# Kernel tuning notes

Measured on AMD Instinct MI355X. Metric: run time of the kernel, lower is better.

## Reference

```python
import jax, jax.numpy as jnp
import numpy as np

B, T, H_IMG, HID, ACT = 128, 100, 72, 512, 2


def _conv(x, w, b, stride, pad):
    y = jax.lax.conv_general_dilated(
        x, w, (stride, stride), [(pad, pad), (pad, pad)],
        dimension_numbers=('NCHW', 'OIHW', 'NCHW'))
    return y + b[None, :, None, None]


def _encode(images, cw1, cb1, cw2, cb2, cw3, cb3, fw1, fb1, fw2, fb2, fw3, fb3):
    relu = jax.nn.relu
    x = relu(_conv(images, cw1, cb1, 3, 2))   # [B,64,24,24]
    x = relu(_conv(x, cw2, cb2, 3, 2))        # [B,64,9,9]
    x = relu(_conv(x, cw3, cb3, 3, 2))        # [B,64,4,4]
    x = x.reshape(x.shape[0], -1)             # [B,1024]
    x = relu(x @ fw1.T + fb1)
    x = relu(x @ fw2.T + fb2)
    return x @ fw3.T + fb3                    # [B,512]


def _gru(actions, h0, w_ih, w_hh, b_ih, b_hh):
    # precompute input projections for all steps: [T,B,3H]
    gi = jnp.einsum('btd,gd->tbg', actions, w_ih) + b_ih

    def step(h, gi_t):
        gh = h @ w_hh.T + b_hh
        i_r, i_i, i_n = jnp.split(gi_t, 3, axis=-1)
        h_r, h_i, h_n = jnp.split(gh, 3, axis=-1)
        r = jax.nn.sigmoid(i_r + h_r)
        z = jax.nn.sigmoid(i_i + h_i)
        n = jnp.tanh(i_n + r * h_n)
        hy = n + z * (h - n)
        return hy, hy

    hT, outs = jax.lax.scan(step, h0, gi)
    return jnp.transpose(outs, (1, 0, 2)), hT  # batch_first output


def setup_inputs() -> dict:
    key = jax.random.key(0)
    ks = jax.random.split(key, 16)
    s = 0.05
    return {
        'images': jax.random.normal(ks[0], (B, 3, H_IMG, H_IMG), jnp.float32),
        'actions': jax.random.normal(ks[1], (B, T, ACT), jnp.float32),
        'cw1': jax.random.normal(ks[2], (64, 3, 5, 5), jnp.float32) * s,
        'cb1': jax.random.normal(ks[3], (64,), jnp.float32) * s,
        'cw2': jax.random.normal(ks[4], (64, 64, 3, 3), jnp.float32) * s,
        'cb2': jax.random.normal(ks[5], (64,), jnp.float32) * s,
        'cw3': jax.random.normal(ks[6], (64, 64, 3, 3), jnp.float32) * s,
        'cb3': jax.random.normal(ks[7], (64,), jnp.float32) * s,
        'fw1': jax.random.normal(ks[8], (1024, 1024), jnp.float32) * 0.02,
        'fb1': jax.random.normal(ks[9], (1024,), jnp.float32) * 0.02,
        'fw2': jax.random.normal(ks[10], (512, 1024), jnp.float32) * 0.02,
        'fb2': jax.random.normal(ks[11], (512,), jnp.float32) * 0.02,
        'fw3': jax.random.normal(ks[12], (512, 512), jnp.float32) * 0.02,
        'fb3': jax.random.normal(ks[13], (512,), jnp.float32) * 0.02,
        'w_ih': jax.random.normal(ks[14], (3 * HID, ACT), jnp.float32) * 0.05,
        'w_hh': jax.random.normal(ks[15], (3 * HID, HID), jnp.float32) * 0.04,
        'b_ih': jnp.zeros((3 * HID,), jnp.float32),
        'b_hh': jnp.zeros((3 * HID,), jnp.float32),
    }


def reference(images, actions, cw1, cb1, cw2, cb2, cw3, cb3,
              fw1, fb1, fw2, fb2, fw3, fb3, w_ih, w_hh, b_ih, b_hh):
    # Encode the start image to a 512-d representation (BigBasicConv),
    # then integrate the action sequence with the hand-rolled GRU,
    # initial hidden state = start representation.
    h0 = _encode(images, cw1, cb1, cw2, cb2, cw3, cb3,
                 fw1, fb1, fw2, fb2, fw3, fb3)
    output, hT = _gru(actions, h0, w_ih, w_hh, b_ih, b_hh)
    return output, hT
```

## Files before the change

kernel.cpp:

```cpp
#include <hip/hip_runtime.h>
#include <cstdint>

#define BB   128
#define TT   100
#define HID  512

typedef __attribute__((ext_vector_type(4))) float f32x4;
typedef __attribute__((ext_vector_type(2))) float f32x2;
typedef __attribute__((ext_vector_type(8))) short short8;
typedef __attribute__((ext_vector_type(4))) short short4_t;

__device__ __forceinline__ short f2bf(float x) {
  unsigned u = __float_as_uint(x);
  unsigned r = (u + 0x7fffu + ((u >> 16) & 1u)) >> 16;
  return (short)r;
}
__device__ __forceinline__ float bf2f(short s) {
  return __uint_as_float(((unsigned)(unsigned short)s) << 16);
}

__global__ __launch_bounds__(256) void wsplit_k(const float* __restrict__ w,
                                                unsigned short* __restrict__ hi,
                                                unsigned short* __restrict__ lo,
                                                int nq) {
  int i = blockIdx.x * 256 + threadIdx.x;
  const int stride = gridDim.x * 256;
  for (; i < nq; i += stride) {
    f32x4 v = *(const f32x4*)(w + 4 * (long)i);
    short4_t h, l;
    #pragma unroll
    for (int c = 0; c < 4; c++) {
      short hh = f2bf(v[c]); h[c] = hh; l[c] = f2bf(v[c] - bf2f(hh));
    }
    *(short4_t*)(hi + 4 * (long)i) = h;
    *(short4_t*)(lo + 4 * (long)i) = l;
  }
}


__global__ __launch_bounds__(192) void conv1_k(const float* __restrict__ in,
                                               const float* __restrict__ w,
                                               const float* __restrict__ bias,
                                               float* __restrict__ out) {
  const int b = blockIdx.x / 24, oy = blockIdx.x % 24;
  __shared__ __attribute__((aligned(16))) float in_s[3][5][76];
  __shared__ __attribute__((aligned(16))) float ws[64][76];
  const int tid = threadIdx.x;
  for (int i = tid; i < 3 * 5 * 76; i += 192) {
    int ic = i / 380, rem = i % 380, r = rem / 76, p = rem % 76;
    int iy = oy * 3 + r - 2, ix = p - 2;
    in_s[ic][r][p] = (iy >= 0 && iy < 72 && ix >= 0 && ix < 72)
                       ? in[((long)(b * 3 + ic) * 72 + iy) * 72 + ix] : 0.f;
  }
  for (int i = tid; i < 64 * 75; i += 192) ws[i / 75][i % 75] = w[i];
  __syncthreads();

  const int ox2 = tid % 12;
  const int og = tid / 12;
  float strip[15][8];
  #pragma unroll
  for (int ic = 0; ic < 3; ic++)
    #pragma unroll
    for (int ky = 0; ky < 5; ky++) {
      const float* bp = &in_s[ic][ky][6 * ox2];
      #pragma unroll
      for (int h = 0; h < 4; h++) {
        f32x2 u = *(const f32x2*)(bp + 2 * h);
        strip[ic * 5 + ky][2 * h] = u[0];
        strip[ic * 5 + ky][2 * h + 1] = u[1];
      }
    }

  #pragma unroll
  for (int j = 0; j < 4; j++) {
    const int oc = og + 16 * j;
    float s0 = bias[oc], s1 = bias[oc];
    const float* wrow = ws[oc];
    #pragma unroll
    for (int k4 = 0; k4 < 18; k4++) {
      f32x4 wq = *(const f32x4*)(wrow + 4 * k4);
      #pragma unroll
      for (int q = 0; q < 4; q++) {
        const int k = 4 * k4 + q, i5 = k / 5, kx = k % 5;
        s0 += strip[i5][kx] * wq[q];
        s1 += strip[i5][kx + 3] * wq[q];
      }
    }
    s0 += strip[14][2] * wrow[72]; s1 += strip[14][5] * wrow[72];
    s0 += strip[14][3] * wrow[73]; s1 += strip[14][6] * wrow[73];
    s0 += strip[14][4] * wrow[74]; s1 += strip[14][7] * wrow[74];
    long o = ((long)(b * 64 + oc) * 24 + oy) * 24 + 2 * ox2;
    out[o] = fmaxf(s0, 0.f);
    out[o + 1] = fmaxf(s1, 0.f);
  }
}

template <int IC, int IH, int IW, int OC, int OH, int OW>
__global__ void convs3(const float* __restrict__ in, const float* __restrict__ w,
                       const float* __restrict__ bias, float* __restrict__ out) {
  const int b = blockIdx.x / OH, oy = blockIdx.x % OH;
  constexpr int PW = 3 * OW;
  constexpr int NT = (OC / 2) * OW;
  __shared__ __attribute__((aligned(16))) float in_s[8][3][PW];
  __shared__ __attribute__((aligned(16))) float w_s[OC][100];
  const int tid = threadIdx.x;
  const int oc = tid / OW, ox = tid % OW;
  float s0 = bias[oc], s1 = bias[oc + OC / 2];
  for (int cc = 0; cc < IC; cc += 8) {
    __syncthreads();
    for (int i = tid; i < 8 * 3 * PW; i += NT) {
      int ic = i / (3 * PW), r = (i / PW) % 3, p = i % PW;
      int iy = oy * 3 - 2 + r, ix = p - 2;
      in_s[ic][r][p] = (iy >= 0 && iy < IH && ix >= 0 && ix < IW)
                         ? in[((long)(b * IC + cc + ic) * IH + iy) * IW + ix] : 0.f;
    }
    for (int i = tid; i < OC * 8 * 9; i += NT) {
      int o = i / 72, r = i % 72;
      w_s[o][(r / 9) * 12 + (r % 9)] = w[(long)(o * IC + cc + r / 9) * 9 + r % 9];
    }
    __syncthreads();
    #pragma unroll
    for (int ic = 0; ic < 8; ic++) {
      const float* wr0 = &w_s[oc][ic * 12];
      const float* wr1 = &w_s[oc + OC / 2][ic * 12];
      f32x4 wa = *(const f32x4*)wr0, wb = *(const f32x4*)(wr0 + 4);
      f32x4 va = *(const f32x4*)wr1, vb = *(const f32x4*)(wr1 + 4);
      float wA[9] = {wa[0], wa[1], wa[2], wa[3], wb[0], wb[1], wb[2], wb[3], wr0[8]};
      float wB[9] = {va[0], va[1], va[2], va[3], vb[0], vb[1], vb[2], vb[3], wr1[8]};
      #pragma unroll
      for (int ky = 0; ky < 3; ky++)
        #pragma unroll
        for (int kx = 0; kx < 3; kx++) {
          float iv = in_s[ic][ky][ox * 3 + kx];
          s0 += iv * wA[ky * 3 + kx];
          s1 += iv * wB[ky * 3 + kx];
        }
    }
  }
  out[((long)(b * OC + oc) * OH + oy) * OW + ox] = fmaxf(s0, 0.f);
  out[((long)(b * OC + oc + OC / 2) * OH + oy) * OW + ox] = fmaxf(s1, 0.f);
}

template <int K, int N, bool RELU>
__global__ __launch_bounds__(128) void fc_mfma(const float* __restrict__ A,
                                               const unsigned short* __restrict__ wh,
                                               const unsigned short* __restrict__ wl,
                                               const float* __restrict__ bias,
                                               float* __restrict__ C) {
  const int nb = N / 32;
  const int rb = (blockIdx.x / nb) * 16, cb = (blockIdx.x % nb) * 32;
  __shared__ __attribute__((aligned(16))) short A_hi[16][K + 8];
  __shared__ __attribute__((aligned(16))) short A_lo[16][K + 8];
  const int tid = threadIdx.x;
  const int wv = tid >> 6, lane = tid & 63, n16 = lane & 15, quad = lane >> 4;

  for (int i = tid; i < 16 * (K / 4); i += 128) {
    int row = i / (K / 4), q = i % (K / 4);
    f32x4 v = *(const f32x4*)(A + (long)(rb + row) * K + 4 * q);
    short4_t sh, sl;
    #pragma unroll
    for (int c = 0; c < 4; c++) {
      short hh = f2bf(v[c]); sh[c] = hh; sl[c] = f2bf(v[c] - bf2f(hh));
    }
    *(short4_t*)&A_hi[row][4 * q] = sh;
    *(short4_t*)&A_lo[row][4 * q] = sl;
  }
  __syncthreads();

  const int col = cb + wv * 16 + n16;
  f32x4 a0 = {0.f, 0.f, 0.f, 0.f}, a1 = a0, a2 = a0;
  constexpr int NP = K / 512;
  #pragma unroll 1
  for (int p = 0; p < NP; p++) {
    short8 fh[16], fl[16];
    const unsigned short* wb0 = wh + (long)col * K + p * 512 + quad * 8;
    const unsigned short* wb1 = wl + (long)col * K + p * 512 + quad * 8;
    #pragma unroll
    for (int ks = 0; ks < 16; ks++) {
      fh[ks] = *(const short8*)(wb0 + ks * 32);
      fl[ks] = *(const short8*)(wb1 + ks * 32);
    }
    #pragma unroll
    for (int ks = 0; ks < 16; ks++) {
      short8 ah = *(const short8*)&A_hi[n16][p * 512 + ks * 32 + quad * 8];
      short8 al = *(const short8*)&A_lo[n16][p * 512 + ks * 32 + quad * 8];
      a0 = __builtin_amdgcn_mfma_f32_16x16x32_bf16(ah, fh[ks], a0, 0, 0, 0);
      a1 = __builtin_amdgcn_mfma_f32_16x16x32_bf16(al, fh[ks], a1, 0, 0, 0);
      a2 = __builtin_amdgcn_mfma_f32_16x16x32_bf16(ah, fl[ks], a2, 0, 0, 0);
    }
  }
  const float bv = bias[col];
  #pragma unroll
  for (int r = 0; r < 4; r++) {
    float v = a0[r] + a1[r] + a2[r] + bv;
    if (RELU) v = fmaxf(v, 0.f);
    C[(long)(rb + quad * 4 + r) * N + col] = v;
  }
}

__global__ __launch_bounds__(192, 1) void gru_k(
    const float* __restrict__ actions, const float* __restrict__ w_ih,
    const float* __restrict__ w_hh, const float* __restrict__ b_ih,
    const float* __restrict__ b_hh, const float* __restrict__ h0,
    float* __restrict__ out, float* __restrict__ hT, unsigned* __restrict__ bar) {
  const int bg = blockIdx.x >> 5;
  const int hg = blockIdx.x & 31;
  const int tid = threadIdx.x;
  const int wv = tid >> 6;
  const int lane = tid & 63;
  const int n16 = lane & 15;
  const int quad = lane >> 4;

  __shared__ short h_hi[16][520];
  __shared__ short h_lo[16][520];
  __shared__ float act_s[16][2 * TT];
  __shared__ float gh_s[3][16][17];
  __shared__ float bih_s[48], bhh_s[48], wih0_s[48], wih1_s[48];

  short8 whi[16], wlo[16];
  {
    const int grow = wv * HID + hg * 16 + n16;
    const float* wr = w_hh + (long)grow * HID + quad * 8;
    #pragma unroll
    for (int ks = 0; ks < 16; ks++) {
      f32x4 v0 = *(const f32x4*)(wr + ks * 32);
      f32x4 v1 = *(const f32x4*)(wr + ks * 32 + 4);
      short8 hi, lo;
      #pragma unroll
      for (int j = 0; j < 4; j++) {
        short h1 = f2bf(v0[j]); hi[j] = h1;     lo[j] = f2bf(v0[j] - bf2f(h1));
        short h2 = f2bf(v1[j]); hi[j + 4] = h2; lo[j + 4] = f2bf(v1[j] - bf2f(h2));
      }
      whi[ks] = hi; wlo[ks] = lo;
    }
  }
  for (int i = tid; i < 48; i += 192) {
    int row = (i >> 4) * HID + hg * 16 + (i & 15);
    bih_s[i] = b_ih[row];
    bhh_s[i] = b_hh[row];
    wih0_s[i] = w_ih[row * 2];
    wih1_s[i] = w_ih[row * 2 + 1];
  }
  for (int i = tid; i < 16 * 2 * TT; i += 192) {
    int m = i / (2 * TT), r = i % (2 * TT);
    act_s[m][r] = actions[(long)(bg * 16 + m) * (2 * TT) + r];
  }
  for (int i = tid; i < 2048; i += 192) {
    int m = i >> 7, k4 = (i & 127) << 2;
    f32x4 v = *(const f32x4*)(h0 + (long)(bg * 16 + m) * HID + k4);
    short4_t sh, sl;
    #pragma unroll
    for (int c2 = 0; c2 < 4; c2++) {
      short hh = f2bf(v[c2]); sh[c2] = hh; sl[c2] = f2bf(v[c2] - bf2f(hh));
    }
    *(short4_t*)&h_hi[m][k4] = sh;
    *(short4_t*)&h_lo[m][k4] = sl;
  }
  __syncthreads();

  unsigned* my_bar = bar + bg * 32;

  #pragma unroll 1
  for (int t = 0; t < TT; t++) {
    f32x4 a0 = {0.f, 0.f, 0.f, 0.f}, a1 = a0, a2 = a0;
    #pragma unroll
    for (int ks = 0; ks < 16; ks++) {
      short8 ah = *(const short8*)&h_hi[n16][ks * 32 + quad * 8];
      short8 al = *(const short8*)&h_lo[n16][ks * 32 + quad * 8];
      a0 = __builtin_amdgcn_mfma_f32_16x16x32_bf16(ah, whi[ks], a0, 0, 0, 0);
      a1 = __builtin_amdgcn_mfma_f32_16x16x32_bf16(al, whi[ks], a1, 0, 0, 0);
      a2 = __builtin_amdgcn_mfma_f32_16x16x32_bf16(ah, wlo[ks], a2, 0, 0, 0);
    }
    #pragma unroll
    for (int r = 0; r < 4; r++)
      gh_s[wv][quad * 4 + r][n16] = a0[r] + a1[r] + a2[r];
    __syncthreads();

    if (tid < 128) {
      const int m = tid >> 3;
      const int n0 = (tid & 7) << 1;
      const float x0 = act_s[m][2 * t], x1 = act_s[m][2 * t + 1];
      float hy[2];
      #pragma unroll
      for (int q = 0; q < 2; q++) {
        int n = n0 + q;
        float hr = gh_s[0][m][n] + bhh_s[n];
        float hz = gh_s[1][m][n] + bhh_s[16 + n];
        float hn = gh_s[2][m][n] + bhh_s[32 + n];
        float ir = x0 * wih0_s[n]      + x1 * wih1_s[n]      + bih_s[n];
        float iz = x0 * wih0_s[16 + n] + x1 * wih1_s[16 + n] + bih_s[16 + n];
        float in_ = x0 * wih0_s[32 + n] + x1 * wih1_s[32 + n] + bih_s[32 + n];
        float rg = 1.f / (1.f + __expf(-(ir + hr)));
        float zg = 1.f / (1.f + __expf(-(iz + hz)));
        float nx = in_ + rg * hn;
        float ng = 1.f - 2.f / (__expf(2.f * nx) + 1.f);
        float hprev = bf2f(h_hi[m][hg * 16 + n]) + bf2f(h_lo[m][hg * 16 + n]);
        hy[q] = ng + zg * (hprev - ng);
      }
      unsigned long long pack = (unsigned long long)__float_as_uint(hy[0]) |
                                ((unsigned long long)__float_as_uint(hy[1]) << 32);
      __hip_atomic_store(
          (unsigned long long*)&out[((long)(bg * 16 + m) * TT + t) * HID + hg * 16 + n0],
          pack, __ATOMIC_RELAXED, __HIP_MEMORY_SCOPE_AGENT);
      if (t == TT - 1)
        *(unsigned long long*)&hT[(long)(bg * 16 + m) * HID + hg * 16 + n0] = pack;
    }
    __syncthreads();

    if (t < TT - 1) {
      if (tid == 0) {
        const unsigned target = 32u * (unsigned)(t + 1);
        unsigned prev = __hip_atomic_fetch_add(my_bar, 1u, __ATOMIC_RELAXED,
                                               __HIP_MEMORY_SCOPE_AGENT);
        if (prev + 1u < target) {
          while (__hip_atomic_load(my_bar, __ATOMIC_RELAXED,
                                   __HIP_MEMORY_SCOPE_AGENT) < target)
            __builtin_amdgcn_s_sleep(1);
        }
      }
      __syncthreads();
      unsigned long long vbuf[22];
      #pragma unroll
      for (int u = 0; u < 21; u++) {
        int i = tid + u * 192;
        int m = i >> 8, j = (i & 255) << 1;
        vbuf[u] = __hip_atomic_load(
            (const unsigned long long*)(out + ((long)(bg * 16 + m) * TT + t) * HID + j),
            __ATOMIC_RELAXED, __HIP_MEMORY_SCOPE_AGENT);
      }
      if (tid < 64) {
        int i = 4032 + tid;
        int m = i >> 8, j = (i & 255) << 1;
        vbuf[21] = __hip_atomic_load(
            (const unsigned long long*)(out + ((long)(bg * 16 + m) * TT + t) * HID + j),
            __ATOMIC_RELAXED, __HIP_MEMORY_SCOPE_AGENT);
      }
      #pragma unroll
      for (int u = 0; u < 21; u++) {
        int i = tid + u * 192;
        int m = i >> 8, j = (i & 255) << 1;
        unsigned long long v = vbuf[u];
        float f0 = __uint_as_float((unsigned)v);
        float f1 = __uint_as_float((unsigned)(v >> 32));
        short s0 = f2bf(f0);
        h_hi[m][j] = s0; h_lo[m][j] = f2bf(f0 - bf2f(s0));
        short s1 = f2bf(f1);
        h_hi[m][j + 1] = s1; h_lo[m][j + 1] = f2bf(f1 - bf2f(s1));
      }
      if (tid < 64) {
        int i = 4032 + tid;
        int m = i >> 8, j = (i & 255) << 1;
        unsigned long long v = vbuf[21];
        float f0 = __uint_as_float((unsigned)v);
        float f1 = __uint_as_float((unsigned)(v >> 32));
        short s0 = f2bf(f0);
        h_hi[m][j] = s0; h_lo[m][j] = f2bf(f0 - bf2f(s0));
        short s1 = f2bf(f1);
        h_hi[m][j + 1] = s1; h_lo[m][j + 1] = f2bf(f1 - bf2f(s1));
      }
      __syncthreads();
    }
  }
}

extern "C" void kernel_launch(void* const* d_in, const int* in_sizes, int n_in,
                              void* d_out, int out_size, void* d_ws, size_t ws_size,
                              hipStream_t stream) {
  const float* images  = (const float*)d_in[0];
  const float* actions = (const float*)d_in[1];
  const float* cw1 = (const float*)d_in[2];
  const float* cb1 = (const float*)d_in[3];
  const float* cw2 = (const float*)d_in[4];
  const float* cb2 = (const float*)d_in[5];
  const float* cw3 = (const float*)d_in[6];
  const float* cb3 = (const float*)d_in[7];
  const float* fw1 = (const float*)d_in[8];
  const float* fb1 = (const float*)d_in[9];
  const float* fw2 = (const float*)d_in[10];
  const float* fb2 = (const float*)d_in[11];
  const float* fw3 = (const float*)d_in[12];
  const float* fb3 = (const float*)d_in[13];
  const float* w_ih = (const float*)d_in[14];
  const float* w_hh = (const float*)d_in[15];
  const float* b_ih = (const float*)d_in[16];
  const float* b_hh = (const float*)d_in[17];

  char* ws = (char*)d_ws;
  unsigned* bar = (unsigned*)ws;
  float* a1 = (float*)(ws + 1024);
  float* a2 = a1 + (long)128 * 64 * 576;
  float* a3 = a2 + (long)128 * 64 * 81;
  float* f1 = a3 + (long)128 * 1024;
  float* f2 = f1 + (long)128 * 1024;
  float* h0 = f2 + (long)128 * 512;
  unsigned short* wfh1 = (unsigned short*)(h0 + 65536);
  unsigned short* wfl1 = wfh1 + (long)1048576;
  unsigned short* wfh2 = wfl1 + (long)1048576;
  unsigned short* wfl2 = wfh2 + (long)524288;
  unsigned short* wfh3 = wfl2 + (long)524288;
  unsigned short* wfl3 = wfh3 + (long)262144;

  float* out = (float*)d_out;
  float* hT  = out + (long)BB * TT * HID;

  hipMemsetAsync(bar, 0, 1024, stream);
  wsplit_k<<<256, 256, 0, stream>>>(fw1, wfh1, wfl1, 262144);
  wsplit_k<<<128, 256, 0, stream>>>(fw2, wfh2, wfl2, 131072);
  wsplit_k<<<64, 256, 0, stream>>>(fw3, wfh3, wfl3, 65536);
  conv1_k<<<128 * 24, 192, 0, stream>>>(images, cw1, cb1, a1);
  convs3<64, 24, 24, 64, 9, 9><<<128 * 9, 288, 0, stream>>>(a1, cw2, cb2, a2);
  convs3<64, 9, 9, 64, 4, 4><<<128 * 4, 128, 0, stream>>>(a2, cw3, cb3, a3);
  fc_mfma<1024, 1024, true><<<256, 128, 0, stream>>>(a3, wfh1, wfl1, fb1, f1);
  fc_mfma<1024, 512, true><<<128, 128, 0, stream>>>(f1, wfh2, wfl2, fb2, f2);
  fc_mfma<512, 512, false><<<128, 128, 0, stream>>>(f2, wfh3, wfl3, fb3, h0);
  gru_k<<<256, 192, 0, stream>>>(actions, w_ih, w_hh, b_ih, b_hh, h0, out, hT, bar);
}
```

Measured before the change: 645.1 us.

## Split GRU split-bf16 products across waves and halve the block count

```diff
diff --git a/kernel.cpp b/kernel.cpp
--- a/kernel.cpp
+++ b/kernel.cpp
@@ -9,6 +9,7 @@
 typedef __attribute__((ext_vector_type(2))) float f32x2;
 typedef __attribute__((ext_vector_type(8))) short short8;
 typedef __attribute__((ext_vector_type(4))) short short4_t;
+typedef unsigned long long ull;
 
 __device__ __forceinline__ short f2bf(float x) {
   unsigned u = __float_as_uint(x);
@@ -198,15 +199,17 @@
   }
 }
 
-__global__ __launch_bounds__(192, 1) void gru_k(
+__global__ __launch_bounds__(384, 1) void gru_k(
     const float* __restrict__ actions, const float* __restrict__ w_ih,
     const float* __restrict__ w_hh, const float* __restrict__ b_ih,
     const float* __restrict__ b_hh, const float* __restrict__ h0,
     float* __restrict__ out, float* __restrict__ hT, unsigned* __restrict__ bar) {
-  const int bg = blockIdx.x >> 5;
-  const int hg = blockIdx.x & 31;
+  const int bg = blockIdx.x >> 4;
+  const int hg = blockIdx.x & 15;
   const int tid = threadIdx.x;
   const int wv = tid >> 6;
+  const int ch = wv % 3;
+  const int sub = wv / 3;
   const int lane = tid & 63;
   const int n16 = lane & 15;
   const int quad = lane >> 4;
@@ -214,38 +217,43 @@
   __shared__ short h_hi[16][520];
   __shared__ short h_lo[16][520];
   __shared__ float act_s[16][2 * TT];
-  __shared__ float gh_s[3][16][17];
-  __shared__ float bih_s[48], bhh_s[48], wih0_s[48], wih1_s[48];
-
-  short8 whi[16], wlo[16];
+  __shared__ float gh_s[3][16][97];
+  __shared__ float bih_s[96], bhh_s[96], wih0_s[96], wih1_s[96];
+
+  short8 wfrag[3][16];
   {
-    const int grow = wv * HID + hg * 16 + n16;
-    const float* wr = w_hh + (long)grow * HID + quad * 8;
-    #pragma unroll
-    for (int ks = 0; ks < 16; ks++) {
-      f32x4 v0 = *(const f32x4*)(wr + ks * 32);
-      f32x4 v1 = *(const f32x4*)(wr + ks * 32 + 4);
-      short8 hi, lo;
-      #pragma unroll
-      for (int j = 0; j < 4; j++) {
-        short h1 = f2bf(v0[j]); hi[j] = h1;     lo[j] = f2bf(v0[j] - bf2f(h1));
-        short h2 = f2bf(v1[j]); hi[j + 4] = h2; lo[j + 4] = f2bf(v1[j] - bf2f(h2));
-      }
-      whi[ks] = hi; wlo[ks] = lo;
-    }
-  }
-  for (int i = tid; i < 48; i += 192) {
-    int row = (i >> 4) * HID + hg * 16 + (i & 15);
+    #pragma unroll
+    for (int g = 0; g < 3; g++) {
+      const int grow = g * HID + hg * 32 + sub * 16 + n16;
+      const float* wr = w_hh + (long)grow * HID + quad * 8;
+      #pragma unroll
+      for (int ks = 0; ks < 16; ks++) {
+        f32x4 v0 = *(const f32x4*)(wr + ks * 32);
+        f32x4 v1 = *(const f32x4*)(wr + ks * 32 + 4);
+        short8 f;
+        #pragma unroll
+        for (int j = 0; j < 4; j++) {
+          float x0 = v0[j], x1 = v1[j];
+          short hh0 = f2bf(x0), hh1 = f2bf(x1);
+          f[j]     = (ch == 2) ? f2bf(x0 - bf2f(hh0)) : hh0;
+          f[j + 4] = (ch == 2) ? f2bf(x1 - bf2f(hh1)) : hh1;
+        }
+        wfrag[g][ks] = f;
+      }
+    }
+  }
+  for (int i = tid; i < 96; i += 384) {
+    int row = (i >> 5) * HID + hg * 32 + (i & 31);
     bih_s[i] = b_ih[row];
     bhh_s[i] = b_hh[row];
     wih0_s[i] = w_ih[row * 2];
     wih1_s[i] = w_ih[row * 2 + 1];
   }
-  for (int i = tid; i < 16 * 2 * TT; i += 192) {
+  for (int i = tid; i < 16 * 2 * TT; i += 384) {
     int m = i / (2 * TT), r = i % (2 * TT);
     act_s[m][r] = actions[(long)(bg * 16 + m) * (2 * TT) + r];
   }
-  for (int i = tid; i < 2048; i += 192) {
+  for (int i = tid; i < 2048; i += 384) {
     int m = i >> 7, k4 = (i & 127) << 2;
     f32x4 v = *(const f32x4*)(h0 + (long)(bg * 16 + m) * HID + k4);
     short4_t sh, sl;
@@ -256,60 +264,70 @@
     *(short4_t*)&h_hi[m][k4] = sh;
     *(short4_t*)&h_lo[m][k4] = sl;
   }
+  float hp0 = 0.f, hp1 = 0.f;
+  if (tid < 256) {
+    const int m = tid >> 4, n0 = (tid & 15) << 1;
+    f32x2 u = *(const f32x2*)(h0 + (long)(bg * 16 + m) * HID + hg * 32 + n0);
+    hp0 = u[0]; hp1 = u[1];
+  }
   __syncthreads();
 
   unsigned* my_bar = bar + bg * 32;
+  short (*hp)[520] = (ch == 1) ? h_lo : h_hi;
 
   #pragma unroll 1
   for (int t = 0; t < TT; t++) {
     f32x4 a0 = {0.f, 0.f, 0.f, 0.f}, a1 = a0, a2 = a0;
     #pragma unroll
     for (int ks = 0; ks < 16; ks++) {
-      short8 ah = *(const short8*)&h_hi[n16][ks * 32 + quad * 8];
-      short8 al = *(const short8*)&h_lo[n16][ks * 32 + quad * 8];
-      a0 = __builtin_amdgcn_mfma_f32_16x16x32_bf16(ah, whi[ks], a0, 0, 0, 0);
-      a1 = __builtin_amdgcn_mfma_f32_16x16x32_bf16(al, whi[ks], a1, 0, 0, 0);
-      a2 = __builtin_amdgcn_mfma_f32_16x16x32_bf16(ah, wlo[ks], a2, 0, 0, 0);
-    }
-    #pragma unroll
-    for (int r = 0; r < 4; r++)
-      gh_s[wv][quad * 4 + r][n16] = a0[r] + a1[r] + a2[r];
+      short8 av = *(const short8*)&hp[n16][ks * 32 + quad * 8];
+      a0 = __builtin_amdgcn_mfma_f32_16x16x32_bf16(av, wfrag[0][ks], a0, 0, 0, 0);
+      a1 = __builtin_amdgcn_mfma_f32_16x16x32_bf16(av, wfrag[1][ks], a1, 0, 0, 0);
+      a2 = __builtin_amdgcn_mfma_f32_16x16x32_bf16(av, wfrag[2][ks], a2, 0, 0, 0);
+    }
+    #pragma unroll
+    for (int r = 0; r < 4; r++) {
+      gh_s[ch][quad * 4 + r][sub * 16 + n16]      = a0[r];
+      gh_s[ch][quad * 4 + r][32 + sub * 16 + n16] = a1[r];
+      gh_s[ch][quad * 4 + r][64 + sub * 16 + n16] = a2[r];
+    }
     __syncthreads();
 
-    if (tid < 128) {
-      const int m = tid >> 3;
-      const int n0 = (tid & 7) << 1;
+    if (tid < 256) {
+      const int m = tid >> 4;
+      const int n0 = (tid & 15) << 1;
       const float x0 = act_s[m][2 * t], x1 = act_s[m][2 * t + 1];
       float hy[2];
       #pragma unroll
       for (int q = 0; q < 2; q++) {
         int n = n0 + q;
-        float hr = gh_s[0][m][n] + bhh_s[n];
-        float hz = gh_s[1][m][n] + bhh_s[16 + n];
-        float hn = gh_s[2][m][n] + bhh_s[32 + n];
+        float hr = gh_s[0][m][n]      + gh_s[1][m][n]      + gh_s[2][m][n]      + bhh_s[n];
+        float hz = gh_s[0][m][32 + n] + gh_s[1][m][32 + n] + gh_s[2][m][32 + n] + bhh_s[32 + n];
+        float hn = gh_s[0][m][64 + n] + gh_s[1][m][64 + n] + gh_s[2][m][64 + n] + bhh_s[64 + n];
         float ir = x0 * wih0_s[n]      + x1 * wih1_s[n]      + bih_s[n];
-        float iz = x0 * wih0_s[16 + n] + x1 * wih1_s[16 + n] + bih_s[16 + n];
-        float in_ = x0 * wih0_s[32 + n] + x1 * wih1_s[32 + n] + bih_s[32 + n];
+        float iz = x0 * wih0_s[32 + n] + x1 * wih1_s[32 + n] + bih_s[32 + n];
+        float in_ = x0 * wih0_s[64 + n] + x1 * wih1_s[64 + n] + bih_s[64 + n];
         float rg = 1.f / (1.f + __expf(-(ir + hr)));
         float zg = 1.f / (1.f + __expf(-(iz + hz)));
         float nx = in_ + rg * hn;
         float ng = 1.f - 2.f / (__expf(2.f * nx) + 1.f);
-        float hprev = bf2f(h_hi[m][hg * 16 + n]) + bf2f(h_lo[m][hg * 16 + n]);
+        float hprev = q ? hp1 : hp0;
         hy[q] = ng + zg * (hprev - ng);
       }
-      unsigned long long pack = (unsigned long long)__float_as_uint(hy[0]) |
-                                ((unsigned long long)__float_as_uint(hy[1]) << 32);
+      hp0 = hy[0]; hp1 = hy[1];
+      ull pack = (ull)__float_as_uint(hy[0]) |
+                 ((ull)__float_as_uint(hy[1]) << 32);
       __hip_atomic_store(
-          (unsigned long long*)&out[((long)(bg * 16 + m) * TT + t) * HID + hg * 16 + n0],
+          (ull*)&out[((long)(bg * 16 + m) * TT + t) * HID + hg * 32 + n0],
           pack, __ATOMIC_RELAXED, __HIP_MEMORY_SCOPE_AGENT);
       if (t == TT - 1)
-        *(unsigned long long*)&hT[(long)(bg * 16 + m) * HID + hg * 16 + n0] = pack;
+        *(ull*)&hT[(long)(bg * 16 + m) * HID + hg * 32 + n0] = pack;
     }
     __syncthreads();
 
     if (t < TT - 1) {
       if (tid == 0) {
-        const unsigned target = 32u * (unsigned)(t + 1);
+        const unsigned target = 16u * (unsigned)(t + 1);
         unsigned prev = __hip_atomic_fetch_add(my_bar, 1u, __ATOMIC_RELAXED,
                                                __HIP_MEMORY_SCOPE_AGENT);
         if (prev + 1u < target) {
@@ -319,27 +337,27 @@
         }
       }
       __syncthreads();
-      unsigned long long vbuf[22];
-      #pragma unroll
-      for (int u = 0; u < 21; u++) {
-        int i = tid + u * 192;
+      ull vbuf[11];
+      #pragma unroll
+      for (int u = 0; u < 10; u++) {
+        int i = tid + u * 384;
         int m = i >> 8, j = (i & 255) << 1;
         vbuf[u] = __hip_atomic_load(
-            (const unsigned long long*)(out + ((long)(bg * 16 + m) * TT + t) * HID + j),
+            (const ull*)(out + ((long)(bg * 16 + m) * TT + t) * HID + j),
             __ATOMIC_RELAXED, __HIP_MEMORY_SCOPE_AGENT);
       }
-      if (tid < 64) {
-        int i = 4032 + tid;
+      if (tid < 256) {
+        int i = 3840 + tid;
         int m = i >> 8, j = (i & 255) << 1;
-        vbuf[21] = __hip_atomic_load(
-            (const unsigned long long*)(out + ((long)(bg * 16 + m) * TT + t) * HID + j),
+        vbuf[10] = __hip_atomic_load(
+            (const ull*)(out + ((long)(bg * 16 + m) * TT + t) * HID + j),
             __ATOMIC_RELAXED, __HIP_MEMORY_SCOPE_AGENT);
       }
       #pragma unroll
-      for (int u = 0; u < 21; u++) {
-        int i = tid + u * 192;
+      for (int u = 0; u < 10; u++) {
+        int i = tid + u * 384;
         int m = i >> 8, j = (i & 255) << 1;
-        unsigned long long v = vbuf[u];
+        ull v = vbuf[u];
         float f0 = __uint_as_float((unsigned)v);
         float f1 = __uint_as_float((unsigned)(v >> 32));
         short s0 = f2bf(f0);
@@ -347,10 +365,10 @@
         short s1 = f2bf(f1);
         h_hi[m][j + 1] = s1; h_lo[m][j + 1] = f2bf(f1 - bf2f(s1));
       }
-      if (tid < 64) {
-        int i = 4032 + tid;
+      if (tid < 256) {
+        int i = 3840 + tid;
         int m = i >> 8, j = (i & 255) << 1;
-        unsigned long long v = vbuf[21];
+        ull v = vbuf[10];
         float f0 = __uint_as_float((unsigned)v);
         float f1 = __uint_as_float((unsigned)(v >> 32));
         short s0 = f2bf(f0);
@@ -413,5 +431,5 @@
   fc_mfma<1024, 1024, true><<<256, 128, 0, stream>>>(a3, wfh1, wfl1, fb1, f1);
   fc_mfma<1024, 512, true><<<128, 128, 0, stream>>>(f1, wfh2, wfl2, fb2, f2);
   fc_mfma<512, 512, false><<<128, 128, 0, stream>>>(f2, wfh3, wfl3, fb3, h0);
-  gru_k<<<256, 192, 0, stream>>>(actions, w_ih, w_hh, b_ih, b_hh, h0, out, hT, bar);
-}
+  gru_k<<<128, 384, 0, stream>>>(actions, w_ih, w_hh, b_ih, b_hh, h0, out, hT, bar);
+}
```

Result: slower. 1.105 ms (+71.2%).
